# Kernel tuning notes

Measured on AMD Instinct MI355X. Metric: run time of the kernel, lower is better.

## Reference

```python
import jax, jax.numpy as jnp
import numpy as np

N_RAYS = 65536
N_COARSE = 64
N_FINE = 128


def setup_inputs() -> dict:
    key = jax.random.key(0)
    k0, k1, k2 = jax.random.split(key, 3)
    origins = jax.random.normal(k0, (N_RAYS, 3), dtype=jnp.float32)
    directions = jax.random.normal(k1, (N_RAYS, 3), dtype=jnp.float32)
    near = jnp.full((N_RAYS,), 2.0, dtype=jnp.float32)
    far = jnp.full((N_RAYS,), 6.0, dtype=jnp.float32)
    # coarse-pass weights used for inverse-CDF (PDF) fine sampling
    weights = jax.random.uniform(k2, (N_RAYS, N_COARSE), dtype=jnp.float32)
    return {"origins": origins, "directions": directions, "near": near,
            "far": far, "weights": weights}


def sample_pdf(bins, weights, n_samples):
    """Inverse-CDF sampling. bins: [N, B], weights: [N, B-1] -> [N, n_samples]."""
    w = weights + 1e-5                       # avoid nans / empty bins
    pdf = w / jnp.sum(w, axis=-1, keepdims=True)
    cdf = jnp.cumsum(pdf, axis=-1)
    cdf = jnp.concatenate([jnp.zeros_like(cdf[..., :1]), cdf], axis=-1)  # [N, B]
    # deterministic (perturb=False) uniform samples in [0, 1]
    u = jnp.linspace(0.0, 1.0, n_samples, dtype=cdf.dtype)
    u = jnp.broadcast_to(u, cdf.shape[:-1] + (n_samples,))
    inds = jax.vmap(lambda c, uu: jnp.searchsorted(c, uu, side="right"))(cdf, u)
    below = jnp.clip(inds - 1, 0, cdf.shape[-1] - 1)
    above = jnp.clip(inds, 0, cdf.shape[-1] - 1)
    cdf_b = jnp.take_along_axis(cdf, below, axis=-1)
    cdf_a = jnp.take_along_axis(cdf, above, axis=-1)
    bins_b = jnp.take_along_axis(bins, below, axis=-1)
    bins_a = jnp.take_along_axis(bins, above, axis=-1)
    denom = cdf_a - cdf_b
    denom = jnp.where(denom < 1e-5, jnp.ones_like(denom), denom)
    t = (u - cdf_b) / denom
    return bins_b + t * (bins_a - bins_b)


def reference(origins, directions, near, far, weights):
    # normalize ray directions (RayBundle.__post_init__)
    directions = directions / jnp.linalg.norm(directions, axis=-1, keepdims=True)
    # stratified coarse depths (uniform in depth, perturb=False)
    t = jnp.linspace(0.0, 1.0, N_COARSE, dtype=origins.dtype)
    z_coarse = near[:, None] + (far - near)[:, None] * t          # [N, 64]
    # hierarchical PDF sampling on interval midpoints (NeRF convention)
    mids = 0.5 * (z_coarse[:, 1:] + z_coarse[:, :-1])             # [N, 63]
    z_fine = sample_pdf(mids, weights[:, 1:-1], N_FINE)           # [N, 128]
    # merge + sort by depth (RaySamples.merge / sort_by_depth)
    z = jnp.sort(jnp.concatenate([z_coarse, z_fine], axis=-1), axis=-1)  # [N, 192]
    positions = origins[:, None, :] + z[..., None] * directions[:, None, :]
    view_directions = jnp.broadcast_to(directions[:, None, :], positions.shape)
    d = jnp.diff(z, axis=-1)
    deltas = jnp.concatenate([d, d[:, -1:]], axis=-1)             # last delta repeats
    return positions, view_directions, z, deltas
```

## Files before the change

kernel.cpp:

```cpp
#include <hip/hip_runtime.h>

#define NR 65536
#define RPB 4

typedef float f32x4 __attribute__((ext_vector_type(4)));

#define SCAN_STEP(ctrl, rmask)                                                  \
    do {                                                                        \
        int _t = __builtin_amdgcn_update_dpp(0, __float_as_int(sc),             \
                                             (ctrl), (rmask), 0xf, true);       \
        sc += __int_as_float(_t);                                               \
    } while (0)

__device__ __forceinline__ float coarse_at(int j, float nr, float dnf) {
    return fmaf((float)j * (1.0f / 63.0f), dnf, nr);
}

__global__ __launch_bounds__(256) void ray_sampler_kernel(
    const float* __restrict__ origins,
    const float* __restrict__ directions,
    const float* __restrict__ nearv,
    const float* __restrict__ farv,
    const float* __restrict__ weights,
    float* __restrict__ out)
{
    __shared__ float s_cdf[RPB][64];
    __shared__ float s_fine[RPB][128];
    __shared__ float s_z[RPB][192];

    const int tid  = threadIdx.x;
    const int wv   = tid >> 6;
    const int lane = tid & 63;
    const int r    = blockIdx.x * RPB + wv;

    const float nr  = nearv[r];
    const float dnf = farv[r] - nr;

    float dx = directions[3*r+0];
    float dy = directions[3*r+1];
    float dz = directions[3*r+2];
    const float invn = 1.0f / sqrtf(dx*dx + dy*dy + dz*dz);
    dx *= invn; dy *= invn; dz *= invn;
    const float ox = origins[3*r+0];
    const float oy = origins[3*r+1];
    const float oz = origins[3*r+2];

    float w = 0.0f;
    if (lane < 62) w = weights[(size_t)r*64 + lane + 1] + 1e-5f;
    float sc = w;
    SCAN_STEP(0x111, 0xf);
    SCAN_STEP(0x112, 0xf);
    SCAN_STEP(0x114, 0xf);
    SCAN_STEP(0x118, 0xf);
    SCAN_STEP(0x142, 0xa);
    SCAN_STEP(0x143, 0xc);
    const float total = __int_as_float(__builtin_amdgcn_readlane(__float_as_int(sc), 63));
    const float invT  = 1.0f / total;
    if (lane < 62) s_cdf[wv][lane + 1] = sc * invT;
    if (lane == 62) s_cdf[wv][0] = 0.0f;

    const float* cdf = s_cdf[wv];
    float fv0, fv1;
    #pragma unroll
    for (int sIt = 0; sIt < 2; ++sIt) {
        const int s = lane + sIt * 64;
        const float u = (float)s * (1.0f/127.0f);
        int lo = 0, hi = 63;
        float vb = 0.0f, va = 1.0f;
        #pragma unroll
        for (int it = 0; it < 6; ++it) {
            if (lo < hi) {
                const int mid = (lo + hi) >> 1;
                const float m = cdf[mid];
                if (m <= u) { lo = mid + 1; vb = m; }
                else        { hi = mid;     va = m; }
            }
        }
        const int below = (lo > 0) ? lo - 1 : 0;
        const int above = (lo > 62) ? 62 : lo;
        const float bb = fmaf(((float)below + 0.5f) * (1.0f/63.0f), dnf, nr);
        const float ba = fmaf(((float)above + 0.5f) * (1.0f/63.0f), dnf, nr);
        float den = va - vb;
        if (den < 1e-5f) den = 1.0f;
        const float tt = (u - vb) / den;
        const float fv = bb + tt * (ba - bb);
        s_fine[wv][s] = fv;
        if (sIt == 0) fv0 = fv; else fv1 = fv;
    }

    const float* fine = s_fine[wv];
    {
        const float v = coarse_at(lane, nr, dnf);
        int lo = 0, hi = 128;
        #pragma unroll
        for (int it = 0; it < 8; ++it) {
            if (lo < hi) {
                const int mid = (lo + hi) >> 1;
                if (fine[mid] < v) lo = mid + 1; else hi = mid;
            }
        }
        s_z[wv][lane + lo] = v;
    }
    #pragma unroll
    for (int sIt = 0; sIt < 2; ++sIt) {
        const float v = (sIt == 0) ? fv0 : fv1;
        int lo = 0, hi = 64;
        #pragma unroll
        for (int it = 0; it < 7; ++it) {
            if (lo < hi) {
                const int mid = (lo + hi) >> 1;
                if (coarse_at(mid, nr, dnf) <= v) lo = mid + 1; else hi = mid;
            }
        }
        s_z[wv][lane + sIt * 64 + lo] = v;
    }

    const float* zw = s_z[wv];
    float* posb = out + (size_t)r * 576;
    float* vdb  = out + (size_t)NR * 576  + (size_t)r * 576;
    float* zb   = out + (size_t)NR * 1152 + (size_t)r * 192;
    float* dlb  = out + (size_t)NR * 1344 + (size_t)r * 192;

    if (lane < 48) {
        const f32x4 zq = *reinterpret_cast<const f32x4*>(&zw[4 * lane]);
        const int nx = (lane == 47) ? 190 : (4 * lane + 4);
        const float znx = zw[nx];
        f32x4 dl;
        dl[0] = zq[1] - zq[0];
        dl[1] = zq[2] - zq[1];
        dl[2] = zq[3] - zq[2];
        dl[3] = (lane == 47) ? (zq[3] - zq[2]) : (znx - zq[3]);
        __builtin_nontemporal_store(zq, reinterpret_cast<f32x4*>(zb) + lane);
        __builtin_nontemporal_store(dl, reinterpret_cast<f32x4*>(dlb) + lane);
    }

    f32x4* pos4 = reinterpret_cast<f32x4*>(posb);
    f32x4* vd4  = reinterpret_cast<f32x4*>(vdb);
    const int l3 = lane % 3;
    #pragma unroll
    for (int qi = 0; qi < 3; ++qi) {
        if (qi < 2 || lane < 16) {
            const int q = lane + qi * 64;
            int p = l3 + qi; p -= (p >= 3) ? 3 : 0;
            const int k0 = (4 * q - p) / 3;
            const float z0 = zw[k0];
            const float z1 = zw[k0 + 1];
            f32x4 pv, vv;
            #pragma unroll
            for (int m = 0; m < 4; ++m) {
                int c = p + m; c -= (c >= 3) ? 3 : 0;
                const float dc = (c == 0) ? dx : ((c == 1) ? dy : dz);
                const float oc = (c == 0) ? ox : ((c == 1) ? oy : oz);
                const float zz = (p + m >= 3) ? z1 : z0;
                pv[m] = fmaf(zz, dc, oc);
                vv[m] = dc;
            }
            __builtin_nontemporal_store(pv, pos4 + q);
            __builtin_nontemporal_store(vv, vd4 + q);
        }
    }
}

extern "C" void kernel_launch(void* const* d_in, const int* in_sizes, int n_in,
                              void* d_out, int out_size, void* d_ws, size_t ws_size,
                              hipStream_t stream) {
    const float* origins    = (const float*)d_in[0];
    const float* directions = (const float*)d_in[1];
    const float* nearv      = (const float*)d_in[2];
    const float* farv       = (const float*)d_in[3];
    const float* weights    = (const float*)d_in[4];
    float* out = (float*)d_out;

    dim3 grid(NR / RPB);
    dim3 block(256);
    ray_sampler_kernel<<<grid, block, 0, stream>>>(origins, directions, nearv, farv, weights, out);
}
```

Before: 81.75 us.

## Process 64 rays per block with bulk coalesced LDS staging of inputs

```diff
diff --git a/kernel.cpp b/kernel.cpp
--- a/kernel.cpp
+++ b/kernel.cpp
@@ -1,7 +1,9 @@
 #include <hip/hip_runtime.h>
 
 #define NR 65536
-#define RPB 4
+#define NBLK 1024
+#define RAYS_PER_BLOCK 64
+#define ITERS 16
 
 typedef float f32x4 __attribute__((ext_vector_type(4)));
 
@@ -16,7 +18,7 @@
     return fmaf((float)j * (1.0f / 63.0f), dnf, nr);
 }
 
-__global__ __launch_bounds__(256) void ray_sampler_kernel(
+__global__ __launch_bounds__(256, 4) void ray_sampler_kernel(
     const float* __restrict__ origins,
     const float* __restrict__ directions,
     const float* __restrict__ nearv,
@@ -24,139 +26,160 @@
     const float* __restrict__ weights,
     float* __restrict__ out)
 {
-    __shared__ float s_cdf[RPB][64];
-    __shared__ float s_fine[RPB][128];
-    __shared__ float s_z[RPB][192];
+    __shared__ float s_w[RAYS_PER_BLOCK][64];
+    __shared__ float s_o[RAYS_PER_BLOCK * 3];
+    __shared__ float s_d[RAYS_PER_BLOCK * 3];
+    __shared__ float s_near[RAYS_PER_BLOCK];
+    __shared__ float s_far[RAYS_PER_BLOCK];
+    __shared__ float s_cdf[4][64];
+    __shared__ float s_fine[4][128];
+    __shared__ float s_z[4][192];
 
     const int tid  = threadIdx.x;
     const int wv   = tid >> 6;
     const int lane = tid & 63;
-    const int r    = blockIdx.x * RPB + wv;
-
-    const float nr  = nearv[r];
-    const float dnf = farv[r] - nr;
-
-    float dx = directions[3*r+0];
-    float dy = directions[3*r+1];
-    float dz = directions[3*r+2];
-    const float invn = 1.0f / sqrtf(dx*dx + dy*dy + dz*dz);
-    dx *= invn; dy *= invn; dz *= invn;
-    const float ox = origins[3*r+0];
-    const float oy = origins[3*r+1];
-    const float oz = origins[3*r+2];
-
-    float w = 0.0f;
-    if (lane < 62) w = weights[(size_t)r*64 + lane + 1] + 1e-5f;
-    float sc = w;
-    SCAN_STEP(0x111, 0xf);
-    SCAN_STEP(0x112, 0xf);
-    SCAN_STEP(0x114, 0xf);
-    SCAN_STEP(0x118, 0xf);
-    SCAN_STEP(0x142, 0xa);
-    SCAN_STEP(0x143, 0xc);
-    const float total = __int_as_float(__builtin_amdgcn_readlane(__float_as_int(sc), 63));
-    const float invT  = 1.0f / total;
-    if (lane < 62) s_cdf[wv][lane + 1] = sc * invT;
-    if (lane == 62) s_cdf[wv][0] = 0.0f;
-
-    const float* cdf = s_cdf[wv];
-    float fv0, fv1;
-    #pragma unroll
-    for (int sIt = 0; sIt < 2; ++sIt) {
-        const int s = lane + sIt * 64;
-        const float u = (float)s * (1.0f/127.0f);
-        int lo = 0, hi = 63;
-        float vb = 0.0f, va = 1.0f;
-        #pragma unroll
-        for (int it = 0; it < 6; ++it) {
-            if (lo < hi) {
-                const int mid = (lo + hi) >> 1;
-                const float m = cdf[mid];
-                if (m <= u) { lo = mid + 1; vb = m; }
-                else        { hi = mid;     va = m; }
-            }
-        }
-        const int below = (lo > 0) ? lo - 1 : 0;
-        const int above = (lo > 62) ? 62 : lo;
-        const float bb = fmaf(((float)below + 0.5f) * (1.0f/63.0f), dnf, nr);
-        const float ba = fmaf(((float)above + 0.5f) * (1.0f/63.0f), dnf, nr);
-        float den = va - vb;
-        if (den < 1e-5f) den = 1.0f;
-        const float tt = (u - vb) / den;
-        const float fv = bb + tt * (ba - bb);
-        s_fine[wv][s] = fv;
-        if (sIt == 0) fv0 = fv; else fv1 = fv;
+    const int ray0 = blockIdx.x * RAYS_PER_BLOCK;
+
+    {
+        const f32x4* wsrc = reinterpret_cast<const f32x4*>(weights + (size_t)ray0 * 64);
+        f32x4* wdst = reinterpret_cast<f32x4*>(&s_w[0][0]);
+        #pragma unroll
+        for (int j = 0; j < 4; ++j) wdst[tid + j * 256] = wsrc[tid + j * 256];
+        if (tid < 48)
+            reinterpret_cast<f32x4*>(s_o)[tid] =
+                reinterpret_cast<const f32x4*>(origins + (size_t)ray0 * 3)[tid];
+        else if (tid < 96)
+            reinterpret_cast<f32x4*>(s_d)[tid - 48] =
+                reinterpret_cast<const f32x4*>(directions + (size_t)ray0 * 3)[tid - 48];
+        else if (tid < 112)
+            reinterpret_cast<f32x4*>(s_near)[tid - 96] =
+                reinterpret_cast<const f32x4*>(nearv + ray0)[tid - 96];
+        else if (tid < 128)
+            reinterpret_cast<f32x4*>(s_far)[tid - 112] =
+                reinterpret_cast<const f32x4*>(farv + ray0)[tid - 112];
     }
-
-    const float* fine = s_fine[wv];
-    {
-        const float v = coarse_at(lane, nr, dnf);
-        int lo = 0, hi = 128;
-        #pragma unroll
-        for (int it = 0; it < 8; ++it) {
-            if (lo < hi) {
-                const int mid = (lo + hi) >> 1;
-                if (fine[mid] < v) lo = mid + 1; else hi = mid;
-            }
-        }
-        s_z[wv][lane + lo] = v;
-    }
-    #pragma unroll
-    for (int sIt = 0; sIt < 2; ++sIt) {
-        const float v = (sIt == 0) ? fv0 : fv1;
-        int lo = 0, hi = 64;
-        #pragma unroll
-        for (int it = 0; it < 7; ++it) {
-            if (lo < hi) {
-                const int mid = (lo + hi) >> 1;
-                if (coarse_at(mid, nr, dnf) <= v) lo = mid + 1; else hi = mid;
-            }
-        }
-        s_z[wv][lane + sIt * 64 + lo] = v;
-    }
-
-    const float* zw = s_z[wv];
-    float* posb = out + (size_t)r * 576;
-    float* vdb  = out + (size_t)NR * 576  + (size_t)r * 576;
-    float* zb   = out + (size_t)NR * 1152 + (size_t)r * 192;
-    float* dlb  = out + (size_t)NR * 1344 + (size_t)r * 192;
-
-    if (lane < 48) {
-        const f32x4 zq = *reinterpret_cast<const f32x4*>(&zw[4 * lane]);
-        const int nx = (lane == 47) ? 190 : (4 * lane + 4);
-        const float znx = zw[nx];
-        f32x4 dl;
-        dl[0] = zq[1] - zq[0];
-        dl[1] = zq[2] - zq[1];
-        dl[2] = zq[3] - zq[2];
-        dl[3] = (lane == 47) ? (zq[3] - zq[2]) : (znx - zq[3]);
-        __builtin_nontemporal_store(zq, reinterpret_cast<f32x4*>(zb) + lane);
-        __builtin_nontemporal_store(dl, reinterpret_cast<f32x4*>(dlb) + lane);
-    }
-
-    f32x4* pos4 = reinterpret_cast<f32x4*>(posb);
-    f32x4* vd4  = reinterpret_cast<f32x4*>(vdb);
-    const int l3 = lane % 3;
-    #pragma unroll
-    for (int qi = 0; qi < 3; ++qi) {
-        if (qi < 2 || lane < 16) {
-            const int q = lane + qi * 64;
-            int p = l3 + qi; p -= (p >= 3) ? 3 : 0;
-            const int k0 = (4 * q - p) / 3;
-            const float z0 = zw[k0];
-            const float z1 = zw[k0 + 1];
-            f32x4 pv, vv;
+    __syncthreads();
+
+    for (int i = 0; i < ITERS; ++i) {
+        const int rl = i * 4 + wv;
+        const int r  = ray0 + rl;
+
+        const float nr  = s_near[rl];
+        const float dnf = s_far[rl] - nr;
+        float dx = s_d[3*rl+0], dy = s_d[3*rl+1], dz = s_d[3*rl+2];
+        const float invn = 1.0f / sqrtf(dx*dx + dy*dy + dz*dz);
+        dx *= invn; dy *= invn; dz *= invn;
+        const float ox = s_o[3*rl+0], oy = s_o[3*rl+1], oz = s_o[3*rl+2];
+
+        float w = (lane < 62) ? s_w[rl][lane + 1] + 1e-5f : 0.0f;
+        float sc = w;
+        SCAN_STEP(0x111, 0xf);
+        SCAN_STEP(0x112, 0xf);
+        SCAN_STEP(0x114, 0xf);
+        SCAN_STEP(0x118, 0xf);
+        SCAN_STEP(0x142, 0xa);
+        SCAN_STEP(0x143, 0xc);
+        const float total = __int_as_float(__builtin_amdgcn_readlane(__float_as_int(sc), 63));
+        const float invT  = 1.0f / total;
+        if (lane < 62) s_cdf[wv][lane + 1] = sc * invT;
+        if (lane == 62) s_cdf[wv][0] = 0.0f;
+
+        const float* cdf = s_cdf[wv];
+        float fv0, fv1;
+        #pragma unroll
+        for (int sIt = 0; sIt < 2; ++sIt) {
+            const int s = lane + sIt * 64;
+            const float u = (float)s * (1.0f/127.0f);
+            int lo = 0, hi = 63;
+            float vb = 0.0f, va = 1.0f;
             #pragma unroll
-            for (int m = 0; m < 4; ++m) {
-                int c = p + m; c -= (c >= 3) ? 3 : 0;
-                const float dc = (c == 0) ? dx : ((c == 1) ? dy : dz);
-                const float oc = (c == 0) ? ox : ((c == 1) ? oy : oz);
-                const float zz = (p + m >= 3) ? z1 : z0;
-                pv[m] = fmaf(zz, dc, oc);
-                vv[m] = dc;
-            }
-            __builtin_nontemporal_store(pv, pos4 + q);
-            __builtin_nontemporal_store(vv, vd4 + q);
+            for (int it = 0; it < 6; ++it) {
+                if (lo < hi) {
+                    const int mid = (lo + hi) >> 1;
+                    const float m = cdf[mid];
+                    if (m <= u) { lo = mid + 1; vb = m; }
+                    else        { hi = mid;     va = m; }
+                }
+            }
+            const int below = (lo > 0) ? lo - 1 : 0;
+            const int above = (lo > 62) ? 62 : lo;
+            const float bb = fmaf(((float)below + 0.5f) * (1.0f/63.0f), dnf, nr);
+            const float ba = fmaf(((float)above + 0.5f) * (1.0f/63.0f), dnf, nr);
+            float den = va - vb;
+            if (den < 1e-5f) den = 1.0f;
+            const float tt = (u - vb) / den;
+            const float fv = bb + tt * (ba - bb);
+            s_fine[wv][s] = fv;
+            if (sIt == 0) fv0 = fv; else fv1 = fv;
+        }
+
+        const float* fine = s_fine[wv];
+        {
+            const float v = coarse_at(lane, nr, dnf);
+            int lo = 0, hi = 128;
+            #pragma unroll
+            for (int it = 0; it < 8; ++it) {
+                if (lo < hi) {
+                    const int mid = (lo + hi) >> 1;
+                    if (fine[mid] < v) lo = mid + 1; else hi = mid;
+                }
+            }
+            s_z[wv][lane + lo] = v;
+        }
+        #pragma unroll
+        for (int sIt = 0; sIt < 2; ++sIt) {
+            const float v = (sIt == 0) ? fv0 : fv1;
+            int lo = 0, hi = 64;
+            #pragma unroll
+            for (int it = 0; it < 7; ++it) {
+                if (lo < hi) {
+                    const int mid = (lo + hi) >> 1;
+                    if (coarse_at(mid, nr, dnf) <= v) lo = mid + 1; else hi = mid;
+                }
+            }
+            s_z[wv][lane + sIt * 64 + lo] = v;
+        }
+
+        const float* zw = s_z[wv];
+        float* zb  = out + (size_t)NR * 1152 + (size_t)r * 192;
+        float* dlb = out + (size_t)NR * 1344 + (size_t)r * 192;
+        if (lane < 48) {
+            const f32x4 zq = *reinterpret_cast<const f32x4*>(&zw[4 * lane]);
+            const int nx = (lane == 47) ? 190 : (4 * lane + 4);
+            const float znx = zw[nx];
+            f32x4 dl;
+            dl[0] = zq[1] - zq[0];
+            dl[1] = zq[2] - zq[1];
+            dl[2] = zq[3] - zq[2];
+            dl[3] = (lane == 47) ? (zq[3] - zq[2]) : (znx - zq[3]);
+            __builtin_nontemporal_store(zq, reinterpret_cast<f32x4*>(zb) + lane);
+            __builtin_nontemporal_store(dl, reinterpret_cast<f32x4*>(dlb) + lane);
+        }
+
+        f32x4* pos4 = reinterpret_cast<f32x4*>(out + (size_t)r * 576);
+        f32x4* vd4  = reinterpret_cast<f32x4*>(out + (size_t)NR * 576 + (size_t)r * 576);
+        const int l3 = lane % 3;
+        #pragma unroll
+        for (int qi = 0; qi < 3; ++qi) {
+            if (qi < 2 || lane < 16) {
+                const int q = lane + qi * 64;
+                int p = l3 + qi; p -= (p >= 3) ? 3 : 0;
+                const int k0 = (4 * q - p) / 3;
+                const float z0 = zw[k0];
+                const float z1 = zw[k0 + 1];
+                f32x4 pv, vv;
+                #pragma unroll
+                for (int m = 0; m < 4; ++m) {
+                    int c = p + m; c -= (c >= 3) ? 3 : 0;
+                    const float dc = (c == 0) ? dx : ((c == 1) ? dy : dz);
+                    const float oc = (c == 0) ? ox : ((c == 1) ? oy : oz);
+                    const float zz = (p + m >= 3) ? z1 : z0;
+                    pv[m] = fmaf(zz, dc, oc);
+                    vv[m] = dc;
+                }
+                __builtin_nontemporal_store(pv, pos4 + q);
+                __builtin_nontemporal_store(vv, vd4 + q);
+            }
         }
     }
 }
@@ -171,7 +194,7 @@
     const float* weights    = (const float*)d_in[4];
     float* out = (float*)d_out;
 
-    dim3 grid(NR / RPB);
+    dim3 grid(NBLK);
     dim3 block(256);
     ray_sampler_kernel<<<grid, block, 0, stream>>>(origins, directions, nearv, farv, weights, out);
 }
```

New measurement: 100.7 us. 1.23x slower.
